# Kernel optimization log

Measured on AMD Instinct MI355X. Metric: run time of the kernel, lower is better.

## Reference

```python
import jax, jax.numpy as jnp
import numpy as np

B, NN, HL = 64, 64, 50
IN_DIM, POS_DIM, ATT_DIM = 384, 64, 256
NEWS_DIM = IN_DIM + POS_DIM  # 448


def setup_inputs() -> dict:
    key = jax.random.key(0)
    ks = jax.random.split(key, 8)
    pos_emb = jax.random.uniform(ks[3], (100, POS_DIM), jnp.float32, -0.1, 0.1)
    pos_emb = pos_emb.at[0].set(0.0)  # initialize() zeros row 0
    return {
        "log_vec": jax.random.normal(ks[0], (B, HL, IN_DIM), jnp.float32),
        "log_mask": jax.random.randint(ks[1], (B, HL), 0, 2, jnp.int32),
        "news_vec": jax.random.normal(ks[2], (B, NN, IN_DIM), jnp.float32),
        "pos_emb": pos_emb,
        "W1": jax.random.normal(ks[4], (ATT_DIM, 2 * NEWS_DIM), jnp.float32) * 0.02,
        "b1": jnp.zeros((ATT_DIM,), jnp.float32),
        "W2": jax.random.normal(ks[5], (1, ATT_DIM), jnp.float32) * 0.02,
        "b2": jnp.zeros((1,), jnp.float32),
    }


def reference(log_vec, log_mask, news_vec, pos_emb, W1, b1, W2, b2):
    b, nn_ = news_vec.shape[:2]
    hl = log_mask.shape[1]
    # append position embeddings (row 0 for candidates, rows 1..hl for history)
    nf = jnp.concatenate(
        [news_vec, jnp.broadcast_to(pos_emb[0], (b, nn_, POS_DIM))], axis=-1)   # (B,NN,ND)
    lf = jnp.concatenate(
        [log_vec, jnp.broadcast_to(pos_emb[1:hl + 1], (b, hl, POS_DIM))], axis=-1)  # (B,HL,ND)
    # affine1(cat[news, log]) == news @ Wn^T + log @ Wl^T + b1 (avoids concat)
    Wn, Wl = W1[:, :NEWS_DIM], W1[:, NEWS_DIM:]
    pn = jnp.einsum('bnd,ad->bna', nf, Wn)   # (B,NN,A)
    pl = jnp.einsum('bhd,ad->bha', lf, Wl)   # (B,HL,A)
    h = jnp.tanh(pn[:, :, None, :] + pl[:, None, :, :] + b1)  # (B,NN,HL,A)
    logits = jnp.einsum('bnha,a->bnh', h, W2[0]) + b2[0]      # (B,NN,HL)
    logits = jnp.where(log_mask[:, None, :] == 0, jnp.float32(-1e9), logits)
    attn = jax.nn.softmax(logits, axis=2)
    user_log_vecs = jnp.einsum('bnh,bhd->bnd', attn, lf)      # (B,NN,ND)
    return user_log_vecs, nf
```

## Files before the change

kernel.cpp:

```cpp
#include <hip/hip_runtime.h>
#include <math.h>

typedef unsigned short u16;
typedef unsigned int   u32;

#define B_       64
#define NN_      64
#define HL_      50
#define IN_DIM   384
#define POS_DIM  64
#define ATT_DIM  256
#define NEWS_DIM 448

typedef __attribute__((ext_vector_type(8))) short short8;
typedef __attribute__((ext_vector_type(4))) float f32x4;

#if __has_builtin(__builtin_amdgcn_exp2f)
#define EXP2F(x) __builtin_amdgcn_exp2f(x)
#else
#define EXP2F(x) exp2f(x)
#endif
#if __has_builtin(__builtin_amdgcn_rcpf)
#define RCPF(x) __builtin_amdgcn_rcpf(x)
#else
#define RCPF(x) (1.0f/(x))
#endif

__device__ __forceinline__ u16 f2bf(float f) {
    union { float f; u32 i; } v; v.f = f;
    u32 r = v.i + 0x7fffu + ((v.i >> 16) & 1u);
    return (u16)(r >> 16);
}
__device__ __forceinline__ float bf2f(u16 u) {
    union { u32 i; float f; } v; v.i = ((u32)u) << 16; return v.f;
}
__device__ __forceinline__ uint2 pack4(float4 v) {
    return make_uint2((u32)f2bf(v.x) | ((u32)f2bf(v.y) << 16),
                      (u32)f2bf(v.z) | ((u32)f2bf(v.w) << 16));
}
__device__ __forceinline__ float fast_tanh(float x) {
    float e = EXP2F(x * 2.88539008f);
    return 1.0f - 2.0f * RCPF(1.0f + e);
}

#define C_W   57344u
#define C_NV  393216u
#define C_LG  307200u
#define C_PS  51200u
#define C_NZ  65536u
#define C_TOT (C_W + C_NV + C_LG + C_PS + C_NZ)

__global__ __launch_bounds__(256) void prep_k(
    const float* __restrict__ W1, const float* __restrict__ newsv,
    const float* __restrict__ logv, const float* __restrict__ pos,
    u16* __restrict__ Wbf, u16* __restrict__ nv_bf, u16* __restrict__ lf_bf,
    float* __restrict__ nf)
{
    u32 i = blockIdx.x * 256u + threadIdx.x;
    if (i < C_W) {
        float4 v = *(const float4*)(W1 + (size_t)i * 4u);
        *(uint2*)(Wbf + (size_t)i * 4u) = pack4(v);
        return;
    }
    i -= C_W;
    if (i < C_NV) {
        float4 v = *(const float4*)(newsv + (size_t)i * 4u);
        *(uint2*)(nv_bf + (size_t)i * 4u) = pack4(v);
        u32 e = i * 4u, r = e / IN_DIM, d = e - r * IN_DIM;
        *(float4*)(nf + (size_t)r * NEWS_DIM + d) = v;
        return;
    }
    i -= C_NV;
    if (i < C_LG) {
        float4 v = *(const float4*)(logv + (size_t)i * 4u);
        u32 e = i * 4u, r = e / IN_DIM, d = e - r * IN_DIM;
        *(uint2*)(lf_bf + (size_t)r * NEWS_DIM + d) = pack4(v);
        return;
    }
    i -= C_LG;
    if (i < C_PS) {
        u32 e = i * 4u, r = e / POS_DIM, d = e - r * POS_DIM;
        u32 h = r % HL_;
        float4 v = *(const float4*)(pos + (size_t)(1u + h) * POS_DIM + d);
        *(uint2*)(lf_bf + (size_t)r * NEWS_DIM + IN_DIM + d) = pack4(v);
        return;
    }
    i -= C_PS;
    if (i < C_NZ) {
        u32 e = i * 4u, r = e / POS_DIM, d = e - r * POS_DIM;
        *(float4*)(nf + (size_t)r * NEWS_DIM + IN_DIM + d) = make_float4(0.f, 0.f, 0.f, 0.f);
    }
}

__global__ __launch_bounds__(64) void gemm_k(
    const u16* __restrict__ nv_bf, const u16* __restrict__ lf_bf,
    const u16* __restrict__ Wbf, const float* __restrict__ b1,
    float* __restrict__ pn, float* __restrict__ plT)
{
    int bid = blockIdx.x;
    int lane = threadIdx.x;
    int m = lane & 15, q = lane >> 4;
    bool is_pn = bid < 256;
    int r0, c0, lda, koff, klen;
    const u16* A;
    if (is_pn) { r0 = (bid & 63) * 64;       c0 = (bid >> 6) * 64; A = nv_bf; lda = IN_DIM;   koff = 0;        klen = IN_DIM; }
    else { int b2 = bid - 256; r0 = (b2 % 50) * 64; c0 = (b2 / 50) * 64; A = lf_bf; lda = NEWS_DIM; koff = NEWS_DIM; klen = NEWS_DIM; }

    f32x4 acc[4][4];
#pragma unroll
    for (int a = 0; a < 4; a++)
#pragma unroll
        for (int b = 0; b < 4; b++) acc[a][b] = (f32x4){0.f, 0.f, 0.f, 0.f};

    const u16* Ap = A + (size_t)(r0 + m) * lda + q * 8;
    const u16* Wp = Wbf + (size_t)(c0 + m) * (2 * NEWS_DIM) + koff + q * 8;

    for (int k = 0; k < klen; k += 32) {
        short8 af[4], wf[4];
#pragma unroll
        for (int rt = 0; rt < 4; rt++) af[rt] = *(const short8*)(Ap + rt * 16 * lda + k);
#pragma unroll
        for (int ct = 0; ct < 4; ct++) wf[ct] = *(const short8*)(Wp + ct * 16 * (2 * NEWS_DIM) + k);
#pragma unroll
        for (int rt = 0; rt < 4; rt++)
#pragma unroll
            for (int ct = 0; ct < 4; ct++)
                acc[rt][ct] = __builtin_amdgcn_mfma_f32_16x16x32_bf16(
                    af[rt], wf[ct], acc[rt][ct], 0, 0, 0);
    }
#pragma unroll
    for (int rt = 0; rt < 4; rt++)
#pragma unroll
        for (int ct = 0; ct < 4; ct++)
#pragma unroll
            for (int i = 0; i < 4; i++) {
                int gr = r0 + rt * 16 + q * 4 + i;
                int gc = c0 + ct * 16 + m;
                float v = acc[rt][ct][i];
                if (is_pn) {
                    pn[(size_t)gr * ATT_DIM + gc] = v + b1[gc];
                } else {
                    int bb = gr / HL_, hh = gr - bb * HL_;
                    plT[(size_t)(bb * ATT_DIM + gc) * HL_ + hh] = v;
                }
            }
}

__global__ __launch_bounds__(256) void attn_out_k(
    const float* __restrict__ pn, const float* __restrict__ plT,
    const float* __restrict__ w2, const int* __restrict__ lmask,
    const u16* __restrict__ lf_bf, float* __restrict__ out)
{
    __shared__ float at_s[4][2][64];
    int lane = threadIdx.x & 63;
    int wid = (int)(threadIdx.x >> 6);
    int g = blockIdx.x * 4 + wid;
    int b = g >> 5;
    int n0 = (g & 31) * 2;
    int hl = (lane < HL_) ? lane : (HL_ - 1);
    const float* pr0 = pn + ((size_t)b * NN_ + n0) * ATT_DIM;
    const float* pr1 = pr0 + ATT_DIM;
    const float* pl = plT + (size_t)b * ATT_DIM * HL_ + hl;

    float a00 = 0.f, a01 = 0.f, a10 = 0.f, a11 = 0.f;
#pragma unroll 2
    for (int a = 0; a < ATT_DIM; a += 4) {
        float4 w4 = *(const float4*)(w2 + a);
        float4 p0 = *(const float4*)(pr0 + a);
        float4 p1 = *(const float4*)(pr1 + a);
        float l0 = pl[(a + 0) * HL_];
        float l1 = pl[(a + 1) * HL_];
        float l2 = pl[(a + 2) * HL_];
        float l3 = pl[(a + 3) * HL_];
        a00 = __builtin_fmaf(fast_tanh(p0.x + l0), w4.x, a00);
        a10 = __builtin_fmaf(fast_tanh(p1.x + l0), w4.x, a10);
        a01 = __builtin_fmaf(fast_tanh(p0.y + l1), w4.y, a01);
        a11 = __builtin_fmaf(fast_tanh(p1.y + l1), w4.y, a11);
        a00 = __builtin_fmaf(fast_tanh(p0.z + l2), w4.z, a00);
        a10 = __builtin_fmaf(fast_tanh(p1.z + l2), w4.z, a10);
        a01 = __builtin_fmaf(fast_tanh(p0.w + l3), w4.w, a01);
        a11 = __builtin_fmaf(fast_tanh(p1.w + l3), w4.w, a11);
    }
    float acc0 = a00 + a01, acc1 = a10 + a11;
    int mv = (lane < HL_) ? lmask[b * HL_ + lane] : 0;
    float lg0 = mv ? acc0 : -1e9f;
    float lg1 = mv ? acc1 : -1e9f;
    float mx0 = lg0, mx1 = lg1;
#pragma unroll
    for (int o = 32; o > 0; o >>= 1) {
        mx0 = fmaxf(mx0, __shfl_xor(mx0, o));
        mx1 = fmaxf(mx1, __shfl_xor(mx1, o));
    }
    float e0 = EXP2F((lg0 - mx0) * 1.44269504f);
    float e1 = EXP2F((lg1 - mx1) * 1.44269504f);
    float s0 = e0, s1 = e1;
#pragma unroll
    for (int o = 32; o > 0; o >>= 1) {
        s0 += __shfl_xor(s0, o);
        s1 += __shfl_xor(s1, o);
    }
    at_s[wid][0][lane] = e0 * RCPF(s0);
    at_s[wid][1][lane] = e1 * RCPF(s1);

    const u16* lfb = lf_bf + (size_t)b * HL_ * NEWS_DIM + lane;
    float acc[2][7];
#pragma unroll
    for (int j = 0; j < 7; j++) { acc[0][j] = 0.f; acc[1][j] = 0.f; }
    for (int h = 0; h < HL_; h++) {
        float v0 = at_s[wid][0][h];
        float v1 = at_s[wid][1][h];
        const u16* row = lfb + (size_t)h * NEWS_DIM;
#pragma unroll
        for (int j = 0; j < 7; j++) {
            float lv = bf2f(row[64 * j]);
            acc[0][j] = fmaf(v0, lv, acc[0][j]);
            acc[1][j] = fmaf(v1, lv, acc[1][j]);
        }
    }
    float* o0 = out + ((size_t)b * NN_ + n0) * NEWS_DIM + lane;
#pragma unroll
    for (int j = 0; j < 7; j++) {
        o0[64 * j] = acc[0][j];
        o0[NEWS_DIM + 64 * j] = acc[1][j];
    }
}

extern "C" void kernel_launch(void* const* d_in, const int* in_sizes, int n_in,
                              void* d_out, int out_size, void* d_ws, size_t ws_size,
                              hipStream_t stream) {
    const float* logv  = (const float*)d_in[0];
    const int*   lmask = (const int*)d_in[1];
    const float* newsv = (const float*)d_in[2];
    const float* pos   = (const float*)d_in[3];
    const float* W1    = (const float*)d_in[4];
    const float* b1    = (const float*)d_in[5];
    const float* w2    = (const float*)d_in[6];

    float* out = (float*)d_out;
    float* nf  = out + (size_t)B_ * NN_ * NEWS_DIM;

    char* ws = (char*)d_ws;
    u16*   lf_bf = (u16*)(ws + 0);
    u16*   Wbf   = (u16*)(ws + 2867200);
    u16*   nv_bf = (u16*)(ws + 3325952);
    float* pn    = (float*)(ws + 6471680);
    float* plT   = (float*)(ws + 10665984);

    prep_k    <<<C_TOT / 256, 256, 0, stream>>>(W1, newsv, logv, pos,
                                                Wbf, nv_bf, lf_bf, nf);
    gemm_k    <<<456, 64, 0, stream>>>(nv_bf, lf_bf, Wbf, b1, pn, plT);
    attn_out_k<<<512, 256, 0, stream>>>(pn, plT, w2, lmask, lf_bf, out);
}
```

Baseline: 134.5 us.

## Halve GEMM row tiles and stage plT chunks in LDS for attention

The projection GEMM now uses 32x64 output tiles instead of 64x64, doubling the grid to 912 workgroups to fill more CUs. The attention kernel regroups blocks so all four waves share one batch and cooperatively stage 32-row chunks of plT into shared memory. Each wave then reads its history terms from LDS rather than issuing strided global loads. This adds block-wide barriers per chunk and more GEMM weight reloads in exchange for better occupancy and load reuse.

Measured after the change: 142.0 us. +5.6%, slower.

```diff
diff --git a/kernel.cpp b/kernel.cpp
--- a/kernel.cpp
+++ b/kernel.cpp
@@ -100,15 +100,15 @@
     int bid = blockIdx.x;
     int lane = threadIdx.x;
     int m = lane & 15, q = lane >> 4;
-    bool is_pn = bid < 256;
+    bool is_pn = bid < 512;
     int r0, c0, lda, koff, klen;
     const u16* A;
-    if (is_pn) { r0 = (bid & 63) * 64;       c0 = (bid >> 6) * 64; A = nv_bf; lda = IN_DIM;   koff = 0;        klen = IN_DIM; }
-    else { int b2 = bid - 256; r0 = (b2 % 50) * 64; c0 = (b2 / 50) * 64; A = lf_bf; lda = NEWS_DIM; koff = NEWS_DIM; klen = NEWS_DIM; }
-
-    f32x4 acc[4][4];
-#pragma unroll
-    for (int a = 0; a < 4; a++)
+    if (is_pn) { r0 = (bid >> 2) * 32; c0 = (bid & 3) * 64; A = nv_bf; lda = IN_DIM;   koff = 0;        klen = IN_DIM; }
+    else { int b2 = bid - 512; r0 = (b2 >> 2) * 32; c0 = (b2 & 3) * 64; A = lf_bf; lda = NEWS_DIM; koff = NEWS_DIM; klen = NEWS_DIM; }
+
+    f32x4 acc[2][4];
+#pragma unroll
+    for (int a = 0; a < 2; a++)
 #pragma unroll
         for (int b = 0; b < 4; b++) acc[a][b] = (f32x4){0.f, 0.f, 0.f, 0.f};
 
@@ -116,20 +116,20 @@
     const u16* Wp = Wbf + (size_t)(c0 + m) * (2 * NEWS_DIM) + koff + q * 8;
 
     for (int k = 0; k < klen; k += 32) {
-        short8 af[4], wf[4];
-#pragma unroll
-        for (int rt = 0; rt < 4; rt++) af[rt] = *(const short8*)(Ap + rt * 16 * lda + k);
+        short8 af[2], wf[4];
+#pragma unroll
+        for (int rt = 0; rt < 2; rt++) af[rt] = *(const short8*)(Ap + rt * 16 * lda + k);
 #pragma unroll
         for (int ct = 0; ct < 4; ct++) wf[ct] = *(const short8*)(Wp + ct * 16 * (2 * NEWS_DIM) + k);
 #pragma unroll
-        for (int rt = 0; rt < 4; rt++)
+        for (int rt = 0; rt < 2; rt++)
 #pragma unroll
             for (int ct = 0; ct < 4; ct++)
                 acc[rt][ct] = __builtin_amdgcn_mfma_f32_16x16x32_bf16(
                     af[rt], wf[ct], acc[rt][ct], 0, 0, 0);
     }
 #pragma unroll
-    for (int rt = 0; rt < 4; rt++)
+    for (int rt = 0; rt < 2; rt++)
 #pragma unroll
         for (int ct = 0; ct < 4; ct++)
 #pragma unroll
@@ -151,35 +151,43 @@
     const float* __restrict__ w2, const int* __restrict__ lmask,
     const u16* __restrict__ lf_bf, float* __restrict__ out)
 {
+    __shared__ float pl_s[32][64];
     __shared__ float at_s[4][2][64];
-    int lane = threadIdx.x & 63;
-    int wid = (int)(threadIdx.x >> 6);
-    int g = blockIdx.x * 4 + wid;
-    int b = g >> 5;
-    int n0 = (g & 31) * 2;
-    int hl = (lane < HL_) ? lane : (HL_ - 1);
+    int tid = threadIdx.x;
+    int lane = tid & 63;
+    int wid = tid >> 6;
+    int b = blockIdx.x >> 3;
+    int n0 = ((blockIdx.x & 7) * 4 + wid) * 2;
     const float* pr0 = pn + ((size_t)b * NN_ + n0) * ATT_DIM;
     const float* pr1 = pr0 + ATT_DIM;
-    const float* pl = plT + (size_t)b * ATT_DIM * HL_ + hl;
+    const float* plb = plT + (size_t)b * ATT_DIM * HL_;
 
     float a00 = 0.f, a01 = 0.f, a10 = 0.f, a11 = 0.f;
+    for (int ac = 0; ac < ATT_DIM; ac += 32) {
+        __syncthreads();
+        for (int i = tid; i < 32 * 64; i += 256) {
+            int a = i >> 6, h = i & 63;
+            pl_s[a][h] = (h < HL_) ? plb[(size_t)(ac + a) * HL_ + h] : 0.f;
+        }
+        __syncthreads();
 #pragma unroll 2
-    for (int a = 0; a < ATT_DIM; a += 4) {
-        float4 w4 = *(const float4*)(w2 + a);
-        float4 p0 = *(const float4*)(pr0 + a);
-        float4 p1 = *(const float4*)(pr1 + a);
-        float l0 = pl[(a + 0) * HL_];
-        float l1 = pl[(a + 1) * HL_];
-        float l2 = pl[(a + 2) * HL_];
-        float l3 = pl[(a + 3) * HL_];
-        a00 = __builtin_fmaf(fast_tanh(p0.x + l0), w4.x, a00);
-        a10 = __builtin_fmaf(fast_tanh(p1.x + l0), w4.x, a10);
-        a01 = __builtin_fmaf(fast_tanh(p0.y + l1), w4.y, a01);
-        a11 = __builtin_fmaf(fast_tanh(p1.y + l1), w4.y, a11);
-        a00 = __builtin_fmaf(fast_tanh(p0.z + l2), w4.z, a00);
-        a10 = __builtin_fmaf(fast_tanh(p1.z + l2), w4.z, a10);
-        a01 = __builtin_fmaf(fast_tanh(p0.w + l3), w4.w, a01);
-        a11 = __builtin_fmaf(fast_tanh(p1.w + l3), w4.w, a11);
+        for (int a = 0; a < 32; a += 4) {
+            float4 w4 = *(const float4*)(w2 + ac + a);
+            float4 p0 = *(const float4*)(pr0 + ac + a);
+            float4 p1 = *(const float4*)(pr1 + ac + a);
+            float l0 = pl_s[a + 0][lane];
+            float l1 = pl_s[a + 1][lane];
+            float l2 = pl_s[a + 2][lane];
+            float l3 = pl_s[a + 3][lane];
+            a00 = __builtin_fmaf(fast_tanh(p0.x + l0), w4.x, a00);
+            a10 = __builtin_fmaf(fast_tanh(p1.x + l0), w4.x, a10);
+            a01 = __builtin_fmaf(fast_tanh(p0.y + l1), w4.y, a01);
+            a11 = __builtin_fmaf(fast_tanh(p1.y + l1), w4.y, a11);
+            a00 = __builtin_fmaf(fast_tanh(p0.z + l2), w4.z, a00);
+            a10 = __builtin_fmaf(fast_tanh(p1.z + l2), w4.z, a10);
+            a01 = __builtin_fmaf(fast_tanh(p0.w + l3), w4.w, a01);
+            a11 = __builtin_fmaf(fast_tanh(p1.w + l3), w4.w, a11);
+        }
     }
     float acc0 = a00 + a01, acc1 = a10 + a11;
     int mv = (lane < HL_) ? lmask[b * HL_ + lane] : 0;
@@ -248,6 +256,6 @@
 
     prep_k    <<<C_TOT / 256, 256, 0, stream>>>(W1, newsv, logv, pos,
                                                 Wbf, nv_bf, lf_bf, nf);
-    gemm_k    <<<456, 64, 0, stream>>>(nv_bf, lf_bf, Wbf, b1, pn, plT);
+    gemm_k    <<<912, 64, 0, stream>>>(nv_bf, lf_bf, Wbf, b1, pn, plT);
     attn_out_k<<<512, 256, 0, stream>>>(pn, plT, w2, lmask, lf_bf, out);
 }
```
